# Optimization experiments

Hardware: AMD Instinct MI355X
Metric: run time of the kernel (lower is better)

## Reference

```python
import jax, jax.numpy as jnp
import numpy as np

L = 3        # num_decoder_layers
H = 1024     # num_decoder_hidden (also input_size and embed dim)
V = 100      # num_decoder_tokens (start_symbol = V, embedding has V+1 rows)
O = 1024     # num_joiner_hidden
B = 64       # batch size
U_MAX = 256  # y sequence length; loop runs U_MAX+1 steps


def setup_inputs() -> dict:
    key = jax.random.key(0)
    ks = jax.random.split(key, 10)
    s = 1.0 / np.sqrt(H)  # torch GRUCell init bound
    return {
        "y": jax.random.randint(ks[0], (B, U_MAX), 0, V),
        "U": jax.random.randint(ks[9], (B,), 1, U_MAX + 1),
        "embed": jax.random.normal(ks[1], (V + 1, H), dtype=jnp.float32),
        "W_ih": jax.random.uniform(ks[2], (L, 3 * H, H), minval=-s, maxval=s, dtype=jnp.float32),
        "W_hh": jax.random.uniform(ks[3], (L, 3 * H, H), minval=-s, maxval=s, dtype=jnp.float32),
        "b_ih": jax.random.uniform(ks[4], (L, 3 * H), minval=-s, maxval=s, dtype=jnp.float32),
        "b_hh": jax.random.uniform(ks[5], (L, 3 * H), minval=-s, maxval=s, dtype=jnp.float32),
        "init_state": jax.random.normal(ks[6], (L, H), dtype=jnp.float32),
        "lin_W": jax.random.uniform(ks[7], (O, H), minval=-s, maxval=s, dtype=jnp.float32),
        "lin_b": jax.random.uniform(ks[8], (O,), minval=-s, maxval=s, dtype=jnp.float32),
    }


def gru_cell(x, h, Wih, Whh, bih, bhh):
    # torch.nn.GRUCell math
    gi = x @ Wih.T + bih          # [B, 3H]
    gh = h @ Whh.T + bhh          # [B, 3H]
    i_r, i_z, i_n = jnp.split(gi, 3, axis=-1)
    h_r, h_z, h_n = jnp.split(gh, 3, axis=-1)
    r = jax.nn.sigmoid(i_r + h_r)
    z = jax.nn.sigmoid(i_z + h_z)
    n = jnp.tanh(i_n + r * h_n)
    return (1.0 - z) * n + z * h


def reference(y, U, embed, W_ih, W_hh, b_ih, b_hh, init_state, lin_W, lin_b):
    # U is unused by the original forward's math (only y.shape[1] matters).
    del U
    bsz = y.shape[0]
    start = embed.shape[0] - 1  # start_symbol = num_decoder_tokens
    # tokens at step u: start symbol at u=0, then y[:, u-1]  -> [B, U_max+1]
    tokens = jnp.concatenate([jnp.full((bsz, 1), start, dtype=y.dtype), y], axis=1)
    state0 = jnp.broadcast_to(init_state, (bsz,) + init_state.shape)  # [B, L, H]

    n_layers = W_ih.shape[0]

    def step(state, tok):
        x = embed[tok]  # [B, H]
        new_states = []
        for l in range(n_layers):  # small fixed layer loop
            x = gru_cell(x, state[:, l], W_ih[l], W_hh[l], b_ih[l], b_hh[l])
            new_states.append(x)
            # dropout p=0.5 is identity in eval mode
        state = jnp.stack(new_states, axis=1)  # [B, L, H]
        out = state[:, -1] @ lin_W.T + lin_b   # [B, O]
        return state, out

    _, outs = jax.lax.scan(step, state0, tokens.T)  # outs: [U_max+1, B, O]
    return jnp.transpose(outs, (1, 0, 2))           # [B, U_max+1, O]
```

## Files before the change

### kernel.cpp

```cpp
#include <hip/hip_runtime.h>
#include <hip/hip_cooperative_groups.h>
#include <stdint.h>

namespace cg = cooperative_groups;

typedef unsigned short u16;
typedef unsigned long long u64;
typedef __bf16 b8v __attribute__((ext_vector_type(8)));
typedef float  f4v __attribute__((ext_vector_type(4)));

#define NB      256
#define NSTAGE  260

#define WS_HB16   0UL
#define WS_INIT16 786432UL
#define WS_EMB16  792576UL
#define WS_PWG    1048576UL
#define WS_PWP    38797312UL
#define WS_ARR    40894464UL
#define WS_GCT    40898560UL
#define WS_REL    40898816UL
#define WS_NEED   40902912UL

#define N_GRU_GRP  2359296
#define N_PRJ_GRP  131072
#define N_EMB_GRP  12928
#define N_TOT_GRP  2503680

__device__ __forceinline__ float sigm(float x) { return 1.0f / (1.0f + __expf(-x)); }
__device__ __forceinline__ float tanh_f(float x) {
  float ax = fabsf(x);
  float e = __expf(-2.0f * ax);
  float m = (1.0f - e) / (1.0f + e);
  return x >= 0.0f ? m : -m;
}
__device__ __forceinline__ u16 f2b(float f) {
  union { float f; uint32_t u; } x; x.f = f;
  uint32_t r = x.u + 0x7fffu + ((x.u >> 16) & 1u);
  return (u16)(r >> 16);
}
__device__ __forceinline__ b8v cvt8(f4v lo, f4v hi) {
  b8v v;
  v[0] = (__bf16)lo[0]; v[1] = (__bf16)lo[1]; v[2] = (__bf16)lo[2]; v[3] = (__bf16)lo[3];
  v[4] = (__bf16)hi[0]; v[5] = (__bf16)hi[1]; v[6] = (__bf16)hi[2]; v[7] = (__bf16)hi[3];
  return v;
}

__device__ __forceinline__ b8v gload16(const u16* p) {
  b8v v;
  asm volatile("global_load_dwordx4 %0, %1, off sc0 sc1"
               : "=&v"(v) : "v"(p));
  return v;
}
__device__ __forceinline__ void astore8(u16* p, u16 a, u16 b, u16 c, u16 d) {
  union { u16 s[4]; u64 q; } u;
  u.s[0] = a; u.s[1] = b; u.s[2] = c; u.s[3] = d;
  __hip_atomic_store((u64*)p, u.q, __ATOMIC_RELAXED, __HIP_MEMORY_SCOPE_AGENT);
}
__device__ __forceinline__ int ld_i(const int* p) {
  return __hip_atomic_load(p, __ATOMIC_RELAXED, __HIP_MEMORY_SCOPE_AGENT);
}
__device__ __forceinline__ void st_i(int* p, int v) {
  __hip_atomic_store(p, v, __ATOMIC_RELAXED, __HIP_MEMORY_SCOPE_AGENT);
}

template<int R, int WN>
__device__ __forceinline__ void gru_round(
    b8v (&fr)[3][2][4], const u16* const (&rowp)[4],
    const b8v (&wreg)[3][4][4], f4v (&acc)[3][4])
{
  if (R < 6) {
    #pragma unroll
    for (int tti = 0; tti < 2; ++tti)
      #pragma unroll
      for (int mi = 0; mi < 4; ++mi)
        fr[(R + 2) % 3][tti][mi] = gload16(rowp[mi] + (R + 2) * 64 + tti * 32);
  }
  asm volatile("s_waitcnt vmcnt(%0)" :: "n"(WN));
  __builtin_amdgcn_sched_barrier(0);
  #pragma unroll
  for (int g = 0; g < 3; ++g)
    #pragma unroll
    for (int tti = 0; tti < 2; ++tti)
      #pragma unroll
      for (int mi = 0; mi < 4; ++mi)
        acc[g][mi] = __builtin_amdgcn_mfma_f32_16x16x32_bf16(
            fr[R % 3][tti][mi], wreg[g][R >> 1][(R & 1) * 2 + tti],
            acc[g][mi], 0, 0, 0);
}

template<int R, int WN>
__device__ __forceinline__ void prj_round(
    b8v (&fr)[3][2][4], const u16* const (&rowp)[4],
    const b8v (&wreg)[3][4][4], f4v (&acc)[4])
{
  if (R < 2) {
    #pragma unroll
    for (int tti = 0; tti < 2; ++tti)
      #pragma unroll
      for (int mi = 0; mi < 4; ++mi)
        fr[(R + 2) % 3][tti][mi] = gload16(rowp[mi] + (R + 2) * 64 + tti * 32);
  }
  asm volatile("s_waitcnt vmcnt(%0)" :: "n"(WN));
  __builtin_amdgcn_sched_barrier(0);
  #pragma unroll
  for (int tti = 0; tti < 2; ++tti)
    #pragma unroll
    for (int mi = 0; mi < 4; ++mi)
      acc[mi] = __builtin_amdgcn_mfma_f32_16x16x32_bf16(
          fr[R % 3][tti][mi], wreg[0][R >> 1][(R & 1) * 2 + tti],
          acc[mi], 0, 0, 0);
}

__global__ __launch_bounds__(256) void prep(
    const float* __restrict__ embed, const float* __restrict__ Wih,
    const float* __restrict__ Whh, const float* __restrict__ initS,
    const float* __restrict__ linW, unsigned char* __restrict__ ws)
{
  int idx = blockIdx.x * 256 + threadIdx.x;
  if (idx < 33) *(int*)(ws + WS_ARR + (size_t)idx * 256) = 0;
  if (idx < N_GRU_GRP) {
    int sid = idx >> 11, w = idx & 2047;
    int q = sid % 6, lct = sid / 6;
    int ct = lct & 63, l = lct >> 6;
    int s = w >> 8, tt = (w >> 6) & 3, lane = w & 63;
    int gate = q >> 1, p = q & 1;
    int row = gate * 1024 + ct * 16 + (lane & 15);
    int k0  = s * 128 + tt * 32 + (lane >> 4) * 8;
    const float* src = (p ? Whh : Wih) + (size_t)l * 3145728 + (size_t)row * 1024 + k0;
    *(b8v*)(ws + WS_PWG + (size_t)idx * 16) =
        cvt8(*(const f4v*)src, *(const f4v*)(src + 4));
  } else if (idx < N_GRU_GRP + N_PRJ_GRP) {
    int i2 = idx - N_GRU_GRP;
    int ct = i2 >> 11, w = i2 & 2047;
    int s = w >> 8, tt = (w >> 6) & 3, lane = w & 63;
    int row = ct * 16 + (lane & 15);
    int k0  = s * 128 + tt * 32 + (lane >> 4) * 8;
    const float* src = linW + (size_t)row * 1024 + k0;
    *(b8v*)(ws + WS_PWP + (size_t)i2 * 16) =
        cvt8(*(const f4v*)src, *(const f4v*)(src + 4));
  } else if (idx < N_GRU_GRP + N_PRJ_GRP + N_EMB_GRP) {
    int i3 = idx - (N_GRU_GRP + N_PRJ_GRP);
    const float* src = embed + (size_t)i3 * 8;
    *(b8v*)(ws + WS_EMB16 + (size_t)i3 * 16) =
        cvt8(*(const f4v*)src, *(const f4v*)(src + 4));
  } else if (idx < N_TOT_GRP) {
    int i4 = idx - (N_GRU_GRP + N_PRJ_GRP + N_EMB_GRP);
    const float* src = initS + (size_t)i4 * 8;
    *(b8v*)(ws + WS_INIT16 + (size_t)i4 * 16) =
        cvt8(*(const f4v*)src, *(const f4v*)(src + 4));
  }
}

__global__ __launch_bounds__(256, 1) void dec_fast(
    const int* __restrict__ y,
    const float* __restrict__ bih, const float* __restrict__ bhh,
    const float* __restrict__ initS, const float* __restrict__ linb,
    float* __restrict__ out, unsigned char* __restrict__ ws)
{
  __shared__ __align__(16) float gate_lds[12][64][20];

  const int tid  = threadIdx.x;
  const int bid  = blockIdx.x;
  const int l    = bid >> 6;
  const int ct   = bid & 63;
  const int c0   = ct << 4;
  const int wv   = tid >> 6;
  const int lane = tid & 63;
  const int lq   = lane >> 4;
  const int ln   = lane & 15;
  const int part = wv & 1;
  const int kh   = wv >> 1;

  u16* hb16        = (u16*)(ws + WS_HB16);
  const u16* ini16 = (const u16*)(ws + WS_INIT16);
  const u16* emb16 = (const u16*)(ws + WS_EMB16);

  int* const myarr = (int*)(ws + WS_ARR + (size_t)(bid & 15) * 256);
  int* const gctr  = (int*)(ws + WS_GCT);
  int* const myrel = (int*)(ws + WS_REL + (size_t)(bid & 15) * 256);
  unsigned char* const relb = ws + WS_REL;

  b8v wreg[3][4][4];
  if (l < 3) {
    const unsigned char* wst = ws + WS_PWG + (size_t)(l * 64 + ct) * 196608;
    #pragma unroll
    for (int g = 0; g < 3; ++g)
      #pragma unroll
      for (int si = 0; si < 4; ++si)
        #pragma unroll
        for (int tt = 0; tt < 4; ++tt)
          wreg[g][si][tt] = *(const b8v*)(wst + (size_t)(g * 2 + part) * 32768
                                              + (size_t)(kh * 4 + si) * 4096
                                              + (size_t)tt * 1024 + (size_t)lane * 16);
  } else {
    const unsigned char* wst = ws + WS_PWP + (size_t)ct * 32768;
    #pragma unroll
    for (int si = 0; si < 2; ++si)
      #pragma unroll
      for (int tt = 0; tt < 4; ++tt)
        wreg[0][si][tt] = *(const b8v*)(wst + (size_t)(wv * 2 + si) * 4096
                                            + (size_t)tt * 1024 + (size_t)lane * 16);
  }

  const int eb = tid >> 2;
  const int cc = (tid & 3) << 2;
  const int cg = c0 + cc;
  float hold[4];
  float rb[4], zb[4], ib[4], hbv[4];
  if (l < 3) {
    const float* biL = bih + l * 3072;
    const float* bhL = bhh + l * 3072;
    #pragma unroll
    for (int j = 0; j < 4; ++j) {
      hold[j] = initS[(l << 10) + cg + j];
      rb[j]  = biL[cg + j]        + bhL[cg + j];
      zb[j]  = biL[1024 + cg + j] + bhL[1024 + cg + j];
      ib[j]  = biL[2048 + cg + j];
      hbv[j] = bhL[2048 + cg + j];
    }
  }
  f4v pbias = (f4v){0.f, 0.f, 0.f, 0.f};
  if (l == 3) pbias = *(const f4v*)(linb + cg);

  int tokCur[4] = {100, 100, 100, 100};

  for (int t = 0; t < NSTAGE; ++t) {
    const int u = t - l;
    const bool active = (u >= 0) && (u <= 256);
    const int rp = (t + 1) & 1;
    const int wp = t & 1;
    if (active) {
      if (l < 3) {
        const int koff0 = (kh << 9) + (lq << 3);
        const u16* rowp[4];
        if (part == 0) {
          if (l == 0) {
            #pragma unroll
            for (int mi = 0; mi < 4; ++mi)
              rowp[mi] = emb16 + ((size_t)tokCur[mi] << 10) + koff0;
          } else {
            const u16* xb = hb16 + (((l - 1) * 2 + rp) << 16) + koff0;
            #pragma unroll
            for (int mi = 0; mi < 4; ++mi)
              rowp[mi] = xb + ((mi * 16 + ln) << 10);
          }
        } else {
          if (u == 0) {
            const u16* hb = ini16 + (l << 10) + koff0;
            #pragma unroll
            for (int mi = 0; mi < 4; ++mi) rowp[mi] = hb;
          } else {
            const u16* hb = hb16 + ((l * 2 + rp) << 16) + koff0;
            #pragma unroll
            for (int mi = 0; mi < 4; ++mi)
              rowp[mi] = hb + ((mi * 16 + ln) << 10);
          }
        }

        int tokNext[4];
        const bool wantTok = (l == 0) && (part == 0) && (u < 256);
        if (wantTok) {
          #pragma unroll
          for (int mi = 0; mi < 4; ++mi)
            tokNext[mi] = y[((mi * 16 + ln) << 8) + u];
        }
        __builtin_amdgcn_sched_barrier(0);

        f4v acc[3][4];
        #pragma unroll
        for (int g = 0; g < 3; ++g)
          #pragma unroll
          for (int mi = 0; mi < 4; ++mi)
            acc[g][mi] = (f4v){0.f, 0.f, 0.f, 0.f};

        b8v fr[3][2][4];
        #pragma unroll
        for (int rr = 0; rr < 2; ++rr)
          #pragma unroll
          for (int tti = 0; tti < 2; ++tti)
            #pragma unroll
            for (int mi = 0; mi < 4; ++mi)
              fr[rr][tti][mi] = gload16(rowp[mi] + rr * 64 + tti * 32);

        gru_round<0, 16>(fr, rowp, wreg, acc);
        gru_round<1, 16>(fr, rowp, wreg, acc);
        gru_round<2, 16>(fr, rowp, wreg, acc);
        gru_round<3, 16>(fr, rowp, wreg, acc);
        gru_round<4, 16>(fr, rowp, wreg, acc);
        gru_round<5, 16>(fr, rowp, wreg, acc);
        gru_round<6, 8>(fr, rowp, wreg, acc);
        gru_round<7, 0>(fr, rowp, wreg, acc);

        #pragma unroll
        for (int g = 0; g < 3; ++g)
          #pragma unroll
          for (int mi = 0; mi < 4; ++mi)
            #pragma unroll
            for (int r4 = 0; r4 < 4; ++r4)
              gate_lds[wv * 3 + g][mi * 16 + lq * 4 + r4][ln] = acc[g][mi][r4];
        __syncthreads();

        {
          const f4v v0  = *(const f4v*)&gate_lds[0][eb][cc];
          const f4v v1  = *(const f4v*)&gate_lds[1][eb][cc];
          const f4v v2  = *(const f4v*)&gate_lds[2][eb][cc];
          const f4v v3  = *(const f4v*)&gate_lds[3][eb][cc];
          const f4v v4  = *(const f4v*)&gate_lds[4][eb][cc];
          const f4v v5  = *(const f4v*)&gate_lds[5][eb][cc];
          const f4v v6  = *(const f4v*)&gate_lds[6][eb][cc];
          const f4v v7  = *(const f4v*)&gate_lds[7][eb][cc];
          const f4v v8  = *(const f4v*)&gate_lds[8][eb][cc];
          const f4v v9  = *(const f4v*)&gate_lds[9][eb][cc];
          const f4v v10 = *(const f4v*)&gate_lds[10][eb][cc];
          const f4v v11 = *(const f4v*)&gate_lds[11][eb][cc];
          u16 pk[4];
          #pragma unroll
          for (int j = 0; j < 4; ++j) {
            float rg = sigm(v0[j] + v6[j] + v3[j] + v9[j] + rb[j]);
            float zg = sigm(v1[j] + v7[j] + v4[j] + v10[j] + zb[j]);
            float ng = tanh_f(v2[j] + v8[j] + ib[j] + rg * (v5[j] + v11[j] + hbv[j]));
            float hn = (1.0f - zg) * ng + zg * hold[j];
            hold[j] = hn;
            pk[j] = f2b(hn);
          }
          astore8(hb16 + ((l * 2 + wp) << 16) + (eb << 10) + cg,
                  pk[0], pk[1], pk[2], pk[3]);
        }
        if (wantTok) {
          #pragma unroll
          for (int mi = 0; mi < 4; ++mi) tokCur[mi] = tokNext[mi];
        }
      } else {
        const u16* xb = hb16 + ((4 + rp) << 16) + (wv << 8) + (lq << 3);
        const u16* rowp[4];
        #pragma unroll
        for (int mi = 0; mi < 4; ++mi) rowp[mi] = xb + ((mi * 16 + ln) << 10);

        f4v acc[4];
        #pragma unroll
        for (int mi = 0; mi < 4; ++mi) acc[mi] = (f4v){0.f, 0.f, 0.f, 0.f};

        b8v fr[3][2][4];
        #pragma unroll
        for (int rr = 0; rr < 2; ++rr)
          #pragma unroll
          for (int tti = 0; tti < 2; ++tti)
            #pragma unroll
            for (int mi = 0; mi < 4; ++mi)
              fr[rr][tti][mi] = gload16(rowp[mi] + rr * 64 + tti * 32);

        prj_round<0, 16>(fr, rowp, wreg, acc);
        prj_round<1, 16>(fr, rowp, wreg, acc);
        prj_round<2, 8>(fr, rowp, wreg, acc);
        prj_round<3, 0>(fr, rowp, wreg, acc);

        #pragma unroll
        for (int mi = 0; mi < 4; ++mi)
          #pragma unroll
          for (int r4 = 0; r4 < 4; ++r4)
            gate_lds[wv][mi * 16 + lq * 4 + r4][ln] = acc[mi][r4];
        __syncthreads();

        {
          const f4v s0 = *(const f4v*)&gate_lds[0][eb][cc];
          const f4v s1 = *(const f4v*)&gate_lds[1][eb][cc];
          const f4v s2 = *(const f4v*)&gate_lds[2][eb][cc];
          const f4v s3 = *(const f4v*)&gate_lds[3][eb][cc];
          f4v v = s0 + s1 + s2 + s3 + pbias;
          *(f4v*)(out + (((size_t)(eb * 257 + u)) << 10) + cg) = v;
        }
      }
    }

    if (t + 1 < NSTAGE) {
      __syncthreads();
      if (tid == 0) {
        const int tgt = t + 1;
        int old = __hip_atomic_fetch_add(myarr, 1, __ATOMIC_RELAXED,
                                         __HIP_MEMORY_SCOPE_AGENT);
        if (old + 1 == (tgt << 4)) {
          int gold = __hip_atomic_fetch_add(gctr, 1, __ATOMIC_RELAXED,
                                            __HIP_MEMORY_SCOPE_AGENT);
          if (gold + 1 == (tgt << 4)) {
            #pragma unroll
            for (int r = 0; r < 16; ++r)
              st_i((int*)(relb + (size_t)r * 256), tgt);
          }
        }
        while (ld_i(myrel) < tgt) __builtin_amdgcn_s_sleep(2);
      }
      __syncthreads();
    }
  }
}

__global__ __launch_bounds__(256) void dec_slow(
    const int* __restrict__ y, const float* __restrict__ embed,
    const float* __restrict__ Wih, const float* __restrict__ Whh,
    const float* __restrict__ bih, const float* __restrict__ bhh,
    const float* __restrict__ initS, const float* __restrict__ linW,
    const float* __restrict__ linb, float* __restrict__ out,
    unsigned char* __restrict__ ws)
{
  cg::grid_group grid = cg::this_grid();
  __shared__ b8v a_lds[2048];
  __shared__ float gate_lds[4][64][17];
  __shared__ int tok_lds[64];
  const int tid = threadIdx.x, bid = blockIdx.x;
  const int l = bid >> 6, c0 = (bid & 63) << 4;
  const int wv = tid >> 6, lane = tid & 63, lq = lane >> 4, ln = lane & 15;
  float* hb32 = (float*)ws;
  const int rowoff = (wv == 0) ? c0 : (wv == 1) ? (1024 + c0) : (2048 + c0);
  const size_t wl = (size_t)(l < 3 ? l : 0) * 3072 * 1024;
  const float* WihL = Wih + wl;
  const float* WhhL = Whh + wl;
  for (int t = 0; t < NSTAGE; ++t) {
    const int u = t - l;
    const bool active = (u >= 0) && (u <= 256);
    const int rp = (t + 1) & 1, wp = t & 1;
    if (active) {
      if (l == 0 && tid < 64)
        tok_lds[tid] = (u == 0) ? 100 : y[(tid << 8) + (u - 1)];
      if (l < 3) {
        f4v acc[4];
        #pragma unroll
        for (int mi = 0; mi < 4; ++mi) acc[mi] = (f4v){0.f, 0.f, 0.f, 0.f};
        const float* xbase = (l == 0) ? embed : (hb32 + (((l - 1) * 2 + rp) << 16));
        const float* hbase = hb32 + ((l * 2 + rp) << 16);
        for (int s = 0; s < 8; ++s) {
          __syncthreads();
          #pragma unroll
          for (int i = 0; i < 8; ++i) {
            int g = tid + (i << 8);
            int sec = g >> 10, gg = g & 1023, b = gg & 63, k8 = gg >> 6;
            int koff = (s << 7) + (k8 << 3);
            const float* src;
            if (sec == 0) src = (l == 0) ? embed + ((size_t)tok_lds[b] << 10) + koff
                                         : xbase + (b << 10) + koff;
            else src = (u == 0) ? initS + (l << 10) + koff : hbase + (b << 10) + koff;
            a_lds[((sec << 4) + k8) * 64 + b] = cvt8(*(const f4v*)src, *(const f4v*)(src + 4));
          }
          __syncthreads();
          const int pstart = (wv == 3) ? 1 : 0;
          const int pend = (wv == 2) ? 1 : 2;
          for (int part = pstart; part < pend; ++part) {
            const float* wrow = ((part == 0) ? WihL : WhhL)
                              + (size_t)(rowoff + ln) * 1024 + (s << 7) + (lq << 3);
            #pragma unroll
            for (int tt = 0; tt < 4; ++tt) {
              b8v bf = cvt8(*(const f4v*)(wrow + (tt << 5)), *(const f4v*)(wrow + (tt << 5) + 4));
              int fb = ((part << 4) + (tt << 2) + lq) * 64 + ln;
              #pragma unroll
              for (int mi = 0; mi < 4; ++mi)
                acc[mi] = __builtin_amdgcn_mfma_f32_16x16x32_bf16(a_lds[fb + (mi << 4)], bf, acc[mi], 0, 0, 0);
            }
          }
        }
        #pragma unroll
        for (int mi = 0; mi < 4; ++mi)
          #pragma unroll
          for (int r = 0; r < 4; ++r)
            gate_lds[wv][(mi << 4) + (lq << 2) + r][ln] = acc[mi][r];
        __syncthreads();
        {
          const int b = tid >> 2, cc = (tid & 3) << 2, cg = c0 + cc;
          const float* biL = bih + l * 3072;
          const float* bhL = bhh + l * 3072;
          float hold[4];
          if (u == 0) {
            #pragma unroll
            for (int j = 0; j < 4; ++j) hold[j] = initS[(l << 10) + cg + j];
          } else {
            const float* hp = hb32 + ((size_t)(l * 2 + rp) << 16) + (b << 10) + cg;
            #pragma unroll
            for (int j = 0; j < 4; ++j) hold[j] = hp[j];
          }
          float* o32 = hb32 + ((size_t)(l * 2 + wp) << 16) + (b << 10) + cg;
          #pragma unroll
          for (int j = 0; j < 4; ++j) {
            int c = cg + j;
            float rpre = gate_lds[0][b][cc + j] + biL[c] + bhL[c];
            float zpre = gate_lds[1][b][cc + j] + biL[1024 + c] + bhL[1024 + c];
            float inn = gate_lds[2][b][cc + j] + biL[2048 + c];
            float hnn = gate_lds[3][b][cc + j] + bhL[2048 + c];
            float rg = sigm(rpre), zg = sigm(zpre);
            float ng = tanh_f(inn + rg * hnn);
            o32[j] = (1.0f - zg) * ng + zg * hold[j];
          }
        }
      } else {
        f4v acc1 = (f4v){0.f, 0.f, 0.f, 0.f};
        const float* xbase = hb32 + ((4 + rp) << 16);
        for (int s = 0; s < 8; ++s) {
          __syncthreads();
          #pragma unroll
          for (int i = 0; i < 4; ++i) {
            int g = tid + (i << 8);
            int b = g & 63, k8 = g >> 6;
            const float* src = xbase + (b << 10) + (s << 7) + (k8 << 3);
            a_lds[k8 * 64 + b] = cvt8(*(const f4v*)src, *(const f4v*)(src + 4));
          }
          __syncthreads();
          const float* wrow = linW + (size_t)(c0 + ln) * 1024 + (s << 7) + (lq << 3);
          #pragma unroll
          for (int tt = 0; tt < 4; ++tt) {
            b8v bf = cvt8(*(const f4v*)(wrow + (tt << 5)), *(const f4v*)(wrow + (tt << 5) + 4));
            acc1 = __builtin_amdgcn_mfma_f32_16x16x32_bf16(
                     a_lds[((tt << 2) + lq) * 64 + (wv << 4) + ln], bf, acc1, 0, 0, 0);
          }
        }
        const float bias = linb[c0 + ln];
        #pragma unroll
        for (int r = 0; r < 4; ++r) {
          int b = (wv << 4) + (lq << 2) + r;
          out[((size_t)(b * 257 + u) << 10) + c0 + ln] = acc1[r] + bias;
        }
      }
    }
    grid.sync();
  }
}

extern "C" void kernel_launch(void* const* d_in, const int* in_sizes, int n_in,
                              void* d_out, int out_size, void* d_ws, size_t ws_size,
                              hipStream_t stream) {
  const int* y        = (const int*)d_in[0];
  const float* embed  = (const float*)d_in[2];
  const float* Wih    = (const float*)d_in[3];
  const float* Whh    = (const float*)d_in[4];
  const float* bih    = (const float*)d_in[5];
  const float* bhh    = (const float*)d_in[6];
  const float* initS  = (const float*)d_in[7];
  const float* linW   = (const float*)d_in[8];
  const float* linb   = (const float*)d_in[9];
  float* out = (float*)d_out;
  unsigned char* ws = (unsigned char*)d_ws;

  if (ws_size >= WS_NEED) {
    hipLaunchKernelGGL(prep, dim3(N_TOT_GRP / 256), dim3(256), 0, stream,
                       embed, Wih, Whh, initS, linW, ws);
    hipLaunchKernelGGL(dec_fast, dim3(NB), dim3(256), 0, stream,
                       y, bih, bhh, initS, linb, out, ws);
  } else {
    void* args[] = {(void*)&y, (void*)&embed, (void*)&Wih, (void*)&Whh,
                    (void*)&bih, (void*)&bhh, (void*)&initS, (void*)&linW,
                    (void*)&linb, (void*)&out, (void*)&ws};
    hipLaunchCooperativeKernel((void*)dec_slow, dim3(NB), dim3(256), args, 0, stream);
  }
}
```

Baseline: 2.815 ms.

## Stream GRU weights from global memory each step instead of holding them in registers

GRU blocks no longer keep their 48 bf16 weight fragments resident in VGPRs. Each step they reload weight fragments from the global workspace alongside the activations, using a 4-deep prefetch ring with adjusted waitcnt thresholds. The projection path loads all four activation rounds up front. The spin-wait sleep in the grid barrier is also shortened. The goal is to free registers and deepen the load pipeline, at the cost of extra global or L2 weight traffic on every step.

```diff
diff --git a/kernel.cpp b/kernel.cpp
--- a/kernel.cpp
+++ b/kernel.cpp
@@ -52,6 +52,12 @@
                : "=&v"(v) : "v"(p));
   return v;
 }
+__device__ __forceinline__ b8v wload16(const unsigned char* p) {
+  b8v v;
+  asm volatile("global_load_dwordx4 %0, %1, off"
+               : "=&v"(v) : "v"(p));
+  return v;
+}
 __device__ __forceinline__ void astore8(u16* p, u16 a, u16 b, u16 c, u16 d) {
   union { u16 s[4]; u64 q; } u;
   u.s[0] = a; u.s[1] = b; u.s[2] = c; u.s[3] = d;
@@ -66,16 +72,10 @@
 
 template<int R, int WN>
 __device__ __forceinline__ void gru_round(
-    b8v (&fr)[3][2][4], const u16* const (&rowp)[4],
-    const b8v (&wreg)[3][4][4], f4v (&acc)[3][4])
+    b8v (&fa)[4][2][4], b8v (&fw)[4][3][2],
+    const u16* const (&rowp)[4], const unsigned char* wstW,
+    f4v (&acc)[3][4])
 {
-  if (R < 6) {
-    #pragma unroll
-    for (int tti = 0; tti < 2; ++tti)
-      #pragma unroll
-      for (int mi = 0; mi < 4; ++mi)
-        fr[(R + 2) % 3][tti][mi] = gload16(rowp[mi] + (R + 2) * 64 + tti * 32);
-  }
   asm volatile("s_waitcnt vmcnt(%0)" :: "n"(WN));
   __builtin_amdgcn_sched_barrier(0);
   #pragma unroll
@@ -85,22 +85,27 @@
       #pragma unroll
       for (int mi = 0; mi < 4; ++mi)
         acc[g][mi] = __builtin_amdgcn_mfma_f32_16x16x32_bf16(
-            fr[R % 3][tti][mi], wreg[g][R >> 1][(R & 1) * 2 + tti],
-            acc[g][mi], 0, 0, 0);
-}
-
-template<int R, int WN>
-__device__ __forceinline__ void prj_round(
-    b8v (&fr)[3][2][4], const u16* const (&rowp)[4],
-    const b8v (&wreg)[3][4][4], f4v (&acc)[4])
-{
-  if (R < 2) {
+            fa[R & 3][tti][mi], fw[R & 3][g][tti], acc[g][mi], 0, 0, 0);
+  if (R < 4) {
     #pragma unroll
     for (int tti = 0; tti < 2; ++tti)
       #pragma unroll
       for (int mi = 0; mi < 4; ++mi)
-        fr[(R + 2) % 3][tti][mi] = gload16(rowp[mi] + (R + 2) * 64 + tti * 32);
-  }
+        fa[R & 3][tti][mi] = gload16(rowp[mi] + (R + 4) * 64 + tti * 32);
+    #pragma unroll
+    for (int g = 0; g < 3; ++g)
+      #pragma unroll
+      for (int tti = 0; tti < 2; ++tti)
+        fw[R & 3][g][tti] = wload16(
+            wstW + g * 65536 + ((R + 4) >> 1) * 4096
+                 + (((R + 4) & 1) * 2 + tti) * 1024);
+  }
+}
+
+template<int R, int WN>
+__device__ __forceinline__ void prj_round(
+    b8v (&fr)[4][2][4], const b8v (&wreg)[2][4], f4v (&acc)[4])
+{
   asm volatile("s_waitcnt vmcnt(%0)" :: "n"(WN));
   __builtin_amdgcn_sched_barrier(0);
   #pragma unroll
@@ -108,7 +113,7 @@
     #pragma unroll
     for (int mi = 0; mi < 4; ++mi)
       acc[mi] = __builtin_amdgcn_mfma_f32_16x16x32_bf16(
-          fr[R % 3][tti][mi], wreg[0][R >> 1][(R & 1) * 2 + tti],
+          fr[R][tti][mi], wreg[R >> 1][(R & 1) * 2 + tti],
           acc[mi], 0, 0, 0);
 }
 
@@ -181,26 +186,19 @@
   int* const myrel = (int*)(ws + WS_REL + (size_t)(bid & 15) * 256);
   unsigned char* const relb = ws + WS_REL;
 
-  b8v wreg[3][4][4];
-  if (l < 3) {
-    const unsigned char* wst = ws + WS_PWG + (size_t)(l * 64 + ct) * 196608;
-    #pragma unroll
-    for (int g = 0; g < 3; ++g)
-      #pragma unroll
-      for (int si = 0; si < 4; ++si)
-        #pragma unroll
-        for (int tt = 0; tt < 4; ++tt)
-          wreg[g][si][tt] = *(const b8v*)(wst + (size_t)(g * 2 + part) * 32768
-                                              + (size_t)(kh * 4 + si) * 4096
-                                              + (size_t)tt * 1024 + (size_t)lane * 16);
-  } else {
+  const unsigned char* const wstW =
+      ws + WS_PWG + (size_t)(l * 64 + ct) * 196608
+         + (size_t)part * 32768 + (size_t)kh * 16384 + (size_t)lane * 16;
+
+  b8v wregP[2][4];
+  if (l == 3) {
     const unsigned char* wst = ws + WS_PWP + (size_t)ct * 32768;
     #pragma unroll
     for (int si = 0; si < 2; ++si)
       #pragma unroll
       for (int tt = 0; tt < 4; ++tt)
-        wreg[0][si][tt] = *(const b8v*)(wst + (size_t)(wv * 2 + si) * 4096
-                                            + (size_t)tt * 1024 + (size_t)lane * 16);
+        wregP[si][tt] = *(const b8v*)(wst + (size_t)(wv * 2 + si) * 4096
+                                          + (size_t)tt * 1024 + (size_t)lane * 16);
   }
 
   const int eb = tid >> 2;
@@ -274,23 +272,32 @@
           for (int mi = 0; mi < 4; ++mi)
             acc[g][mi] = (f4v){0.f, 0.f, 0.f, 0.f};
 
-        b8v fr[3][2][4];
-        #pragma unroll
-        for (int rr = 0; rr < 2; ++rr)
+        b8v fa[4][2][4];
+        b8v fw[4][3][2];
+        #pragma unroll
+        for (int rr = 0; rr < 4; ++rr) {
           #pragma unroll
           for (int tti = 0; tti < 2; ++tti)
             #pragma unroll
             for (int mi = 0; mi < 4; ++mi)
-              fr[rr][tti][mi] = gload16(rowp[mi] + rr * 64 + tti * 32);
-
-        gru_round<0, 16>(fr, rowp, wreg, acc);
-        gru_round<1, 16>(fr, rowp, wreg, acc);
-        gru_round<2, 16>(fr, rowp, wreg, acc);
-        gru_round<3, 16>(fr, rowp, wreg, acc);
-        gru_round<4, 16>(fr, rowp, wreg, acc);
-        gru_round<5, 16>(fr, rowp, wreg, acc);
-        gru_round<6, 8>(fr, rowp, wreg, acc);
-        gru_round<7, 0>(fr, rowp, wreg, acc);
+              fa[rr][tti][mi] = gload16(rowp[mi] + rr * 64 + tti * 32);
+          #pragma unroll
+          for (int g = 0; g < 3; ++g)
+            #pragma unroll
+            for (int tti = 0; tti < 2; ++tti)
+              fw[rr][g][tti] = wload16(
+                  wstW + g * 65536 + (rr >> 1) * 4096
+                       + ((rr & 1) * 2 + tti) * 1024);
+        }
+
+        gru_round<0, 42>(fa, fw, rowp, wstW, acc);
+        gru_round<1, 42>(fa, fw, rowp, wstW, acc);
+        gru_round<2, 42>(fa, fw, rowp, wstW, acc);
+        gru_round<3, 42>(fa, fw, rowp, wstW, acc);
+        gru_round<4, 42>(fa, fw, rowp, wstW, acc);
+        gru_round<5, 28>(fa, fw, rowp, wstW, acc);
+        gru_round<6, 14>(fa, fw, rowp, wstW, acc);
+        gru_round<7, 0>(fa, fw, rowp, wstW, acc);
 
         #pragma unroll
         for (int g = 0; g < 3; ++g)
@@ -341,19 +348,19 @@
         #pragma unroll
         for (int mi = 0; mi < 4; ++mi) acc[mi] = (f4v){0.f, 0.f, 0.f, 0.f};
 
-        b8v fr[3][2][4];
-        #pragma unroll
-        for (int rr = 0; rr < 2; ++rr)
+        b8v fr[4][2][4];
+        #pragma unroll
+        for (int rr = 0; rr < 4; ++rr)
           #pragma unroll
           for (int tti = 0; tti < 2; ++tti)
             #pragma unroll
             for (int mi = 0; mi < 4; ++mi)
               fr[rr][tti][mi] = gload16(rowp[mi] + rr * 64 + tti * 32);
 
-        prj_round<0, 16>(fr, rowp, wreg, acc);
-        prj_round<1, 16>(fr, rowp, wreg, acc);
-        prj_round<2, 8>(fr, rowp, wreg, acc);
-        prj_round<3, 0>(fr, rowp, wreg, acc);
+        prj_round<0, 24>(fr, wregP, acc);
+        prj_round<1, 16>(fr, wregP, acc);
+        prj_round<2, 8>(fr, wregP, acc);
+        prj_round<3, 0>(fr, wregP, acc);
 
         #pragma unroll
         for (int mi = 0; mi < 4; ++mi)
@@ -388,7 +395,7 @@
               st_i((int*)(relb + (size_t)r * 256), tgt);
           }
         }
-        while (ld_i(myrel) < tgt) __builtin_amdgcn_s_sleep(2);
+        while (ld_i(myrel) < tgt) __builtin_amdgcn_s_sleep(1);
       }
       __syncthreads();
     }
```

Result: slower. 3.305 ms (+17.4%).
